# Performance work log

Measured on AMD Instinct MI355X. Metric: run time of the kernel, lower is better.

Reference implementation:

```python
import jax, jax.numpy as jnp
import numpy as np

NEG_SLOPE = 0.01  # torch LeakyReLU default


def lrelu(x):
    return jnp.where(x >= 0, x, NEG_SLOPE * x)


def rgcn_layer(x, edge_index, edge_type, W_rel, W_root, b_rgcn):
    """PyG RGCNConv (no bases/blocks, aggr='mean'):
    out = x @ root + bias + sum_r mean_{j in N_r(i)}(x_j) @ W_r
    Single fused gather/segment_sum over relation-interleaved segment ids."""
    N, D = x.shape
    R = W_rel.shape[0]
    src, dst = edge_index[0], edge_index[1]
    seg = dst * R + edge_type  # interleave relation into segment id
    summed = jax.ops.segment_sum(x[src], seg, num_segments=N * R).reshape(N, R, D)
    cnt = jax.ops.segment_sum(jnp.ones(edge_type.shape, x.dtype), seg, num_segments=N * R).reshape(N, R)
    mean = summed / jnp.maximum(cnt, 1.0)[..., None]  # [N, R, D]
    return x @ W_root + b_rgcn + jnp.einsum('nrd,rde->ne', mean, W_rel)


def setup_inputs() -> dict:
    key = jax.random.key(0)
    N, E, D = 100_000, 3_200_000, 128
    q = D // 4
    ks = jax.random.split(key, 24)
    s = 0.02
    inp = {
        'des': jax.random.normal(ks[0], (N, 768), jnp.float32),
        'tweet': jax.random.normal(ks[1], (N, 768), jnp.float32),
        'prop': jax.random.normal(ks[2], (N, 14), jnp.float32),
        'edge_index': jax.random.randint(ks[3], (2, E), 0, N),
        'edge_type': jax.random.randint(ks[4], (E,), 0, 2),
        # feature encoders
        'W_des': jax.random.normal(ks[5], (768, q), jnp.float32) * s,
        'b_des': jnp.zeros((q,), jnp.float32),
        'W_tweet': jax.random.normal(ks[6], (768, q), jnp.float32) * s,
        'b_tweet': jnp.zeros((q,), jnp.float32),
        'W_prop': jax.random.normal(ks[7], (14, q), jnp.float32) * s,
        'b_prop': jnp.zeros((q,), jnp.float32),
        'W_in': jax.random.normal(ks[8], (3 * q, D), jnp.float32) * s,
        'b_in': jnp.zeros((D,), jnp.float32),
        # shared RGCNConv weights (applied twice)
        'W_rel': jax.random.normal(ks[9], (2, D, D), jnp.float32) * s,
        'W_root': jax.random.normal(ks[10], (D, D), jnp.float32) * s,
        'b_rgcn': jnp.zeros((D,), jnp.float32),
        # output head
        'W_o1': jax.random.normal(ks[11], (D, D), jnp.float32) * s,
        'b_o1': jnp.zeros((D,), jnp.float32),
        'W_o2': jax.random.normal(ks[12], (D, 2), jnp.float32) * s,
        'b_o2': jnp.zeros((2,), jnp.float32),
    }
    return inp


def reference(des, tweet, prop, edge_index, edge_type,
              W_des, b_des, W_tweet, b_tweet, W_prop, b_prop,
              W_in, b_in, W_rel, W_root, b_rgcn,
              W_o1, b_o1, W_o2, b_o2):
    d = lrelu(des @ W_des + b_des)
    t = lrelu(tweet @ W_tweet + b_tweet)
    p = lrelu(prop @ W_prop + b_prop)
    x = lrelu(jnp.concatenate([d, t, p], axis=1) @ W_in + b_in)
    x = rgcn_layer(x, edge_index, edge_type, W_rel, W_root, b_rgcn)
    # dropout is identity at eval time
    x = rgcn_layer(x, edge_index, edge_type, W_rel, W_root, b_rgcn)
    x = lrelu(x @ W_o1 + b_o1)
    return jax.nn.softmax(x @ W_o2 + b_o2, axis=1)
```

## Files before the change

kernel.cpp:

```cpp
#include <hip/hip_runtime.h>
#include <math.h>

typedef __bf16 bf16;
typedef bf16  v8bf __attribute__((ext_vector_type(8)));
typedef bf16  v2bf __attribute__((ext_vector_type(2)));
typedef float v4f  __attribute__((ext_vector_type(4)));

#define LB __launch_bounds__(256)

static inline int cdiv(int a, int b){ return (a + b - 1) / b; }


__global__ LB void zero_int(int* __restrict__ p, int n){
  int i = blockIdx.x * 256 + threadIdx.x;
  if (i < n) p[i] = 0;
}

__global__ LB void count_edges(const int* __restrict__ ei, const int* __restrict__ et,
                               int* __restrict__ cnt, int E, int R){
  int e = blockIdx.x * 256 + threadIdx.x;
  if (e >= E) return;
  int dst = ei[E + e];
  int ty  = et[e];
  atomicAdd(&cnt[dst * R + ty], 1);
}

__global__ LB void block_sum_k(const int* __restrict__ cnt, int* __restrict__ bsum, int NS){
  __shared__ int sh[256];
  int t = threadIdx.x;
  int base = blockIdx.x * 1024;
  int s = 0;
  for (int i = t; i < 1024; i += 256){ int g = base + i; if (g < NS) s += cnt[g]; }
  sh[t] = s; __syncthreads();
  for (int d = 128; d > 0; d >>= 1){ if (t < d) sh[t] += sh[t + d]; __syncthreads(); }
  if (t == 0) bsum[blockIdx.x] = sh[0];
}

__global__ LB void scan_bsum_k(int* __restrict__ bsum, int nb){
  __shared__ int sh[256];
  int t = threadIdx.x;
  int v = (t < nb) ? bsum[t] : 0;
  sh[t] = v; __syncthreads();
  for (int d = 1; d < 256; d <<= 1){
    int add = (t >= d) ? sh[t - d] : 0;
    __syncthreads();
    sh[t] += add;
    __syncthreads();
  }
  if (t < nb) bsum[t] = sh[t] - v;
}

__global__ LB void scan_scatter_k(const int* __restrict__ cnt, const int* __restrict__ bsum,
                                  int* __restrict__ off, int* __restrict__ cursor,
                                  float* __restrict__ degInv, int NS){
  __shared__ int sh[256];
  int t = threadIdx.x;
  int base = blockIdx.x * 1024 + t * 4;
  int v[4];
  #pragma unroll
  for (int j = 0; j < 4; ++j){ int g = base + j; v[j] = (g < NS) ? cnt[g] : 0; }
  int tsum = v[0] + v[1] + v[2] + v[3];
  sh[t] = tsum; __syncthreads();
  for (int d = 1; d < 256; d <<= 1){
    int add = (t >= d) ? sh[t - d] : 0;
    __syncthreads();
    sh[t] += add;
    __syncthreads();
  }
  int o = bsum[blockIdx.x] + sh[t] - tsum;
  #pragma unroll
  for (int j = 0; j < 4; ++j){
    int g = base + j;
    if (g < NS){
      off[g] = o;
      cursor[g] = o;
      degInv[g] = 1.0f / (float)(v[j] > 0 ? v[j] : 1);
      o += v[j];
      if (g == NS - 1) off[NS] = o;
    }
  }
}

__global__ LB void fill_edges(const int* __restrict__ ei, const int* __restrict__ et,
                              int* __restrict__ cursor, int* __restrict__ srcS, int E, int R){
  int e = blockIdx.x * 256 + threadIdx.x;
  if (e >= E) return;
  int src = ei[e];
  int dst = ei[E + e];
  int ty  = et[e];
  int pos = atomicAdd(&cursor[dst * R + ty], 1);
  srcS[pos] = src;
}


__global__ LB void agg_mean_k(const bf16* __restrict__ X, const int* __restrict__ srcS,
                              const int* __restrict__ off, const float* __restrict__ degInv,
                              bf16* __restrict__ mean, int NS){
  int w = (int)(((size_t)blockIdx.x * blockDim.x + threadIdx.x) >> 6);
  int lane = threadIdx.x & 63;
  if (w >= NS) return;
  int s0 = off[w], s1 = off[w + 1];
  float ax = 0.f, ay = 0.f;
  int i = s0;
  for (; i + 4 <= s1; i += 4){
    int j0 = srcS[i], j1 = srcS[i + 1], j2 = srcS[i + 2], j3 = srcS[i + 3];
    v2bf u0 = *(const v2bf*)(X + (size_t)j0 * 128 + lane * 2);
    v2bf u1 = *(const v2bf*)(X + (size_t)j1 * 128 + lane * 2);
    v2bf u2 = *(const v2bf*)(X + (size_t)j2 * 128 + lane * 2);
    v2bf u3 = *(const v2bf*)(X + (size_t)j3 * 128 + lane * 2);
    ax += (float)u0[0] + (float)u1[0] + (float)u2[0] + (float)u3[0];
    ay += (float)u0[1] + (float)u1[1] + (float)u2[1] + (float)u3[1];
  }
  for (; i < s1; ++i){
    int j = srcS[i];
    v2bf u = *(const v2bf*)(X + (size_t)j * 128 + lane * 2);
    ax += (float)u[0]; ay += (float)u[1];
  }
  float di = degInv[w];
  v2bf o; o[0] = (bf16)(ax * di); o[1] = (bf16)(ay * di);
  *(v2bf*)(mean + (size_t)w * 128 + lane * 2) = o;
}


__global__ LB void prep_bt(const float* __restrict__ W, bf16* __restrict__ BT,
                           int K, int Nc, int KP){
  int idx = blockIdx.x * 256 + threadIdx.x;
  if (idx >= Nc * KP) return;
  int n = idx / KP, k = idx - n * KP;
  BT[idx] = (k < K) ? (bf16)W[(size_t)k * Nc + n] : (bf16)0.f;
}

__global__ LB void prep_stack(const float* __restrict__ Wroot, const float* __restrict__ Wrel,
                              bf16* __restrict__ BT, int D){
  int KP = 3 * D;
  int idx = blockIdx.x * 256 + threadIdx.x;
  if (idx >= D * KP) return;
  int n = idx / KP, k = idx - n * KP;
  float v = (k < D) ? Wroot[(size_t)k * D + n] : Wrel[(size_t)(k - D) * D + n];
  BT[idx] = (bf16)v;
}


template<int BN, bool LRELU, bool DUALA, bool ABF, bool CBF>
__global__ LB void gemm_mfma(const void* __restrict__ Av, int lda,
                             const void* __restrict__ A2v, int lda2, int KA,
                             const bf16* __restrict__ BT, int KP,
                             void* __restrict__ Cv, int ldc,
                             const float* __restrict__ bias,
                             int M, int K){
  __shared__ __align__(16) bf16 As[64][40];
  __shared__ __align__(16) bf16 Bs[BN][40];
  const int t = threadIdx.x;
  const int row0 = blockIdx.x * 64;
  const int col0 = blockIdx.y * BN;
  const int wv = t >> 6, ln = t & 63;
  const int mr = ln & 15, quad = ln >> 4;
  const int sr = t >> 2;
  const int sc = (t & 3) * 8;

  v4f acc[BN / 16];
  #pragma unroll
  for (int f = 0; f < BN / 16; ++f) acc[f] = (v4f)0.f;

  for (int k0 = 0; k0 < KP; k0 += 32){
    {
      int gr = row0 + sr;
      int gk = k0 + sc;
      bool useA2 = DUALA && (k0 >= KA);
      if (ABF){
        const bf16* src;
        if (useA2) src = (const bf16*)A2v + (size_t)gr * lda2 + (gk - KA);
        else       src = (const bf16*)Av  + (size_t)gr * lda  + gk;
        v8bf val;
        if (gr < M && gk + 8 <= K){
          val = *(const v8bf*)src;
        } else {
          #pragma unroll
          for (int j = 0; j < 8; ++j)
            val[j] = (gr < M && gk + j < K) ? src[j] : (bf16)0.f;
        }
        *(v8bf*)&As[sr][sc] = val;
      } else {
        const float* src;
        if (useA2) src = (const float*)A2v + (size_t)gr * lda2 + (gk - KA);
        else       src = (const float*)Av  + (size_t)gr * lda  + gk;
        bf16 tmp[8];
        if (gr < M && gk + 8 <= K){
          float4 f0 = *(const float4*)src;
          float4 f1 = *(const float4*)(src + 4);
          tmp[0]=(bf16)f0.x; tmp[1]=(bf16)f0.y; tmp[2]=(bf16)f0.z; tmp[3]=(bf16)f0.w;
          tmp[4]=(bf16)f1.x; tmp[5]=(bf16)f1.y; tmp[6]=(bf16)f1.z; tmp[7]=(bf16)f1.w;
        } else {
          #pragma unroll
          for (int j = 0; j < 8; ++j)
            tmp[j] = (gr < M && gk + j < K) ? (bf16)src[j] : (bf16)0.f;
        }
        *(v8bf*)&As[sr][sc] = *(v8bf*)tmp;
      }
    }
    if (BN == 64 || t < 128){
      *(v8bf*)&Bs[sr][sc] = *(const v8bf*)&BT[(size_t)(col0 + sr) * KP + k0 + sc];
    }
    __syncthreads();
    v8bf a = *(v8bf*)&As[wv * 16 + mr][quad * 8];
    #pragma unroll
    for (int f = 0; f < BN / 16; ++f){
      v8bf b = *(v8bf*)&Bs[f * 16 + mr][quad * 8];
      acc[f] = __builtin_amdgcn_mfma_f32_16x16x32_bf16(a, b, acc[f], 0, 0, 0);
    }
    __syncthreads();
  }

  #pragma unroll
  for (int f = 0; f < BN / 16; ++f){
    int gc = col0 + f * 16 + mr;
    float bv = bias[gc];
    #pragma unroll
    for (int r = 0; r < 4; ++r){
      int gr = row0 + wv * 16 + quad * 4 + r;
      if (gr < M){
        float v = acc[f][r] + bv;
        if (LRELU) v = (v >= 0.f) ? v : 0.01f * v;
        if (CBF) ((bf16*)Cv)[(size_t)gr * ldc + gc] = (bf16)v;
        else     ((float*)Cv)[(size_t)gr * ldc + gc] = v;
      }
    }
  }
}


__global__ LB void head_softmax(const bf16* __restrict__ H, const float* __restrict__ Wo2,
                                const float* __restrict__ bo2, float* __restrict__ out, int Nn){
  int gtid = blockIdx.x * 256 + threadIdx.x;
  int node = gtid >> 5;
  int lane = gtid & 31;
  if (node >= Nn) return;
  float l0 = 0.f, l1 = 0.f;
  #pragma unroll
  for (int kk = 0; kk < 4; ++kk){
    int k = lane + kk * 32;
    float h = (float)H[(size_t)node * 128 + k];
    l0 = fmaf(h, Wo2[k * 2 + 0], l0);
    l1 = fmaf(h, Wo2[k * 2 + 1], l1);
  }
  #pragma unroll
  for (int m = 16; m >= 1; m >>= 1){
    l0 += __shfl_xor(l0, m, 64);
    l1 += __shfl_xor(l1, m, 64);
  }
  if (lane == 0){
    l0 += bo2[0]; l1 += bo2[1];
    float mx = fmaxf(l0, l1);
    float e0 = __expf(l0 - mx), e1 = __expf(l1 - mx);
    float inv = 1.f / (e0 + e1);
    out[(size_t)node * 2 + 0] = e0 * inv;
    out[(size_t)node * 2 + 1] = e1 * inv;
  }
}


extern "C" void kernel_launch(void* const* d_in, const int* in_sizes, int n_in,
                              void* d_out, int out_size, void* d_ws, size_t ws_size,
                              hipStream_t stream) {
  const float* des    = (const float*)d_in[0];
  const float* tweet  = (const float*)d_in[1];
  const float* prop   = (const float*)d_in[2];
  const int*   ei     = (const int*)d_in[3];
  const int*   et     = (const int*)d_in[4];
  const float* W_des  = (const float*)d_in[5];
  const float* b_des  = (const float*)d_in[6];
  const float* W_tw   = (const float*)d_in[7];
  const float* b_tw   = (const float*)d_in[8];
  const float* W_pr   = (const float*)d_in[9];
  const float* b_pr   = (const float*)d_in[10];
  const float* W_in   = (const float*)d_in[11];
  const float* b_in   = (const float*)d_in[12];
  const float* W_rel  = (const float*)d_in[13];
  const float* W_root = (const float*)d_in[14];
  const float* b_rg   = (const float*)d_in[15];
  const float* W_o1   = (const float*)d_in[16];
  const float* b_o1   = (const float*)d_in[17];
  const float* W_o2   = (const float*)d_in[18];
  const float* b_o2   = (const float*)d_in[19];

  const int Nn = in_sizes[0] / 768;
  const int E  = in_sizes[4];
  const int q  = in_sizes[6];
  const int D  = in_sizes[12];
  const int R  = in_sizes[13] / (D * D);
  const int NS = Nn * R;
  const int K3 = 3 * q;

  char* p = (char*)d_ws;
  auto carve = [&](size_t bytes) -> void* {
    void* r = (void*)p;
    p += (bytes + 255) & ~(size_t)255;
    return r;
  };
  int*   cnt     = (int*)  carve((size_t)NS * 4);
  int*   off     = (int*)  carve((size_t)(NS + 1) * 4);
  int*   cursor  = (int*)  carve((size_t)NS * 4);
  float* degInv  = (float*)carve((size_t)NS * 4);
  int*   bsum    = (int*)  carve(4096 * 4);
  int*   srcS    = (int*)  carve((size_t)E * 4);
  bf16*  bufA    = (bf16*) carve((size_t)Nn * D * 2);
  bf16*  bufB    = (bf16*) carve((size_t)Nn * D * 2);
  bf16*  mean    = (bf16*) carve((size_t)Nn * R * D * 2);
  bf16*  dtp     = mean;
  bf16*  BT_des  = (bf16*) carve((size_t)q * 768 * 2);
  bf16*  BT_tw   = (bf16*) carve((size_t)q * 768 * 2);
  bf16*  BT_pr   = (bf16*) carve((size_t)q * 32 * 2);
  bf16*  BT_in   = (bf16*) carve((size_t)D * K3 * 2);
  bf16*  BT_st   = (bf16*) carve((size_t)D * 3 * D * 2);
  bf16*  BT_o1   = (bf16*) carve((size_t)D * D * 2);

  const int NB1 = cdiv(NS, 1024);

  zero_int<<<cdiv(NS, 256), 256, 0, stream>>>(cnt, NS);
  count_edges<<<cdiv(E, 256), 256, 0, stream>>>(ei, et, cnt, E, R);
  block_sum_k<<<NB1, 256, 0, stream>>>(cnt, bsum, NS);
  scan_bsum_k<<<1, 256, 0, stream>>>(bsum, NB1);
  scan_scatter_k<<<NB1, 256, 0, stream>>>(cnt, bsum, off, cursor, degInv, NS);
  fill_edges<<<cdiv(E, 256), 256, 0, stream>>>(ei, et, cursor, srcS, E, R);

  prep_bt<<<cdiv(q * 768, 256), 256, 0, stream>>>(W_des, BT_des, 768, q, 768);
  prep_bt<<<cdiv(q * 768, 256), 256, 0, stream>>>(W_tw,  BT_tw,  768, q, 768);
  prep_bt<<<cdiv(q * 32, 256), 256, 0, stream>>>(W_pr,  BT_pr,  14,  q, 32);
  prep_bt<<<cdiv(D * K3, 256), 256, 0, stream>>>(W_in,  BT_in,  K3,  D, K3);
  prep_stack<<<cdiv(D * 3 * D, 256), 256, 0, stream>>>(W_root, W_rel, BT_st, D);
  prep_bt<<<cdiv(D * D, 256), 256, 0, stream>>>(W_o1,  BT_o1,  D,   D, D);

  const int gx = cdiv(Nn, 64);

  gemm_mfma<32, true, false, false, true><<<dim3(gx, 1), 256, 0, stream>>>(
      des, 768, nullptr, 0, 0, BT_des, 768, dtp + 0, K3, b_des, Nn, 768);
  gemm_mfma<32, true, false, false, true><<<dim3(gx, 1), 256, 0, stream>>>(
      tweet, 768, nullptr, 0, 0, BT_tw, 768, dtp + q, K3, b_tw, Nn, 768);
  gemm_mfma<32, true, false, false, true><<<dim3(gx, 1), 256, 0, stream>>>(
      prop, 14, nullptr, 0, 0, BT_pr, 32, dtp + 2 * q, K3, b_pr, Nn, 14);

  gemm_mfma<64, true, false, true, true><<<dim3(gx, 2), 256, 0, stream>>>(
      dtp, K3, nullptr, 0, 0, BT_in, K3, bufA, D, b_in, Nn, K3);

  const int aggGrid = cdiv(NS * 64, 256);

  agg_mean_k<<<aggGrid, 256, 0, stream>>>(bufA, srcS, off, degInv, mean, NS);
  gemm_mfma<64, false, true, true, true><<<dim3(gx, 2), 256, 0, stream>>>(
      bufA, D, mean, R * D, D, BT_st, 3 * D, bufB, D, b_rg, Nn, 3 * D);

  agg_mean_k<<<aggGrid, 256, 0, stream>>>(bufB, srcS, off, degInv, mean, NS);
  gemm_mfma<64, false, true, true, true><<<dim3(gx, 2), 256, 0, stream>>>(
      bufB, D, mean, R * D, D, BT_st, 3 * D, bufA, D, b_rg, Nn, 3 * D);

  gemm_mfma<64, true, false, true, true><<<dim3(gx, 2), 256, 0, stream>>>(
      bufA, D, nullptr, 0, 0, BT_o1, D, bufB, D, b_o1, Nn, D);
  head_softmax<<<cdiv(Nn * 32, 256), 256, 0, stream>>>(bufB, W_o2, b_o2, (float*)d_out, Nn);
}
```

Baseline: 1.429 ms.

## Build CSR via two-level bucket partition instead of global atomics

Replaces the count/scan/fill CSR construction, which does random global atomics per edge, with a two-pass radix-style partition. Edges are first bucketed by dst>>9 using shared-memory histograms and staged writes. Each bucket then builds its segment offsets and the sorted src list with shared-memory atomics. This trades the scattered global atomic traffic for extra passes over the edge arrays and more workspace, and it assumes Nn fits in 256 buckets and R*512 segments fit in SPB (R<=2).

Result: faster. 1.190 ms (-16.7%).

```diff
diff --git a/kernel.cpp b/kernel.cpp
--- a/kernel.cpp
+++ b/kernel.cpp
@@ -11,35 +11,39 @@
 static inline int cdiv(int a, int b){ return (a + b - 1) / b; }
 
 
+#define PNB   256
+#define CHUNK 4096
+#define SPB   1024
+
 __global__ LB void zero_int(int* __restrict__ p, int n){
   int i = blockIdx.x * 256 + threadIdx.x;
   if (i < n) p[i] = 0;
 }
 
-__global__ LB void count_edges(const int* __restrict__ ei, const int* __restrict__ et,
-                               int* __restrict__ cnt, int E, int R){
-  int e = blockIdx.x * 256 + threadIdx.x;
-  if (e >= E) return;
-  int dst = ei[E + e];
-  int ty  = et[e];
-  atomicAdd(&cnt[dst * R + ty], 1);
-}
-
-__global__ LB void block_sum_k(const int* __restrict__ cnt, int* __restrict__ bsum, int NS){
+__global__ LB void bucket_count_k(const int* __restrict__ ei, int* __restrict__ gCnt, int E){
+  __shared__ int lh[PNB];
+  int t = threadIdx.x;
+  int base = blockIdx.x * CHUNK;
+  for (int i = t; i < PNB; i += 256) lh[i] = 0;
+  __syncthreads();
+  #pragma unroll
+  for (int j = 0; j < 16; ++j){
+    int i = base + t + j * 256;
+    if (i < E){
+      int d = ei[E + i];
+      atomicAdd(&lh[d >> 9], 1);
+    }
+  }
+  __syncthreads();
+  for (int i = t; i < PNB; i += 256) if (lh[i]) atomicAdd(&gCnt[i], lh[i]);
+}
+
+__global__ LB void bucket_scan_k(const int* __restrict__ gCnt, int* __restrict__ bucketBase,
+                                 int* __restrict__ gCur, int* __restrict__ off,
+                                 int NBk, int E, int NS){
   __shared__ int sh[256];
   int t = threadIdx.x;
-  int base = blockIdx.x * 1024;
-  int s = 0;
-  for (int i = t; i < 1024; i += 256){ int g = base + i; if (g < NS) s += cnt[g]; }
-  sh[t] = s; __syncthreads();
-  for (int d = 128; d > 0; d >>= 1){ if (t < d) sh[t] += sh[t + d]; __syncthreads(); }
-  if (t == 0) bsum[blockIdx.x] = sh[0];
-}
-
-__global__ LB void scan_bsum_k(int* __restrict__ bsum, int nb){
-  __shared__ int sh[256];
-  int t = threadIdx.x;
-  int v = (t < nb) ? bsum[t] : 0;
+  int v = (t < NBk) ? gCnt[t] : 0;
   sh[t] = v; __syncthreads();
   for (int d = 1; d < 256; d <<= 1){
     int add = (t >= d) ? sh[t - d] : 0;
@@ -47,49 +51,120 @@
     sh[t] += add;
     __syncthreads();
   }
-  if (t < nb) bsum[t] = sh[t] - v;
-}
-
-__global__ LB void scan_scatter_k(const int* __restrict__ cnt, const int* __restrict__ bsum,
-                                  int* __restrict__ off, int* __restrict__ cursor,
-                                  float* __restrict__ degInv, int NS){
-  __shared__ int sh[256];
+  int excl = sh[t] - v;
+  if (t < NBk){ bucketBase[t] = excl; gCur[t] = excl; }
+  if (t == 0){ bucketBase[NBk] = E; off[NS] = E; }
+}
+
+__global__ LB void partition_k(const int* __restrict__ ei, const int* __restrict__ et,
+                               int* __restrict__ gCur,
+                               int* __restrict__ partSrc, int* __restrict__ partSeg,
+                               int E, int R){
+  __shared__ int lh[PNB];
+  __shared__ int lbase[PNB];
+  __shared__ int gb[PNB];
+  __shared__ int stageSrc[CHUNK];
+  __shared__ int stageSeg[CHUNK];
   int t = threadIdx.x;
-  int base = blockIdx.x * 1024 + t * 4;
-  int v[4];
-  #pragma unroll
-  for (int j = 0; j < 4; ++j){ int g = base + j; v[j] = (g < NS) ? cnt[g] : 0; }
-  int tsum = v[0] + v[1] + v[2] + v[3];
-  sh[t] = tsum; __syncthreads();
+  int base = blockIdx.x * CHUNK;
+  int cntE = E - base; if (cntE > CHUNK) cntE = CHUNK;
+  for (int i = t; i < PNB; i += 256) lh[i] = 0;
+  __syncthreads();
+  int seg_[16], src_[16], pk_[16];
+  #pragma unroll
+  for (int j = 0; j < 16; ++j){
+    int i = t + j * 256;
+    if (i < cntE){
+      int e = base + i;
+      int s  = ei[e];
+      int d  = ei[E + e];
+      int ty = et[e];
+      seg_[j] = d * R + ty;
+      src_[j] = s;
+      int b = d >> 9;
+      int r = atomicAdd(&lh[b], 1);
+      pk_[j] = (b << 16) | r;
+    } else pk_[j] = -1;
+  }
+  __syncthreads();
+  int v = lh[t];
+  lbase[t] = v; __syncthreads();
   for (int d = 1; d < 256; d <<= 1){
-    int add = (t >= d) ? sh[t - d] : 0;
-    __syncthreads();
-    sh[t] += add;
-    __syncthreads();
-  }
-  int o = bsum[blockIdx.x] + sh[t] - tsum;
+    int add = (t >= d) ? lbase[t - d] : 0;
+    __syncthreads();
+    lbase[t] += add;
+    __syncthreads();
+  }
+  int excl = lbase[t] - v;
+  int gbase = 0;
+  if (v > 0) gbase = atomicAdd(&gCur[t], v);
+  __syncthreads();
+  lbase[t] = excl;
+  gb[t] = gbase;
+  __syncthreads();
+  #pragma unroll
+  for (int j = 0; j < 16; ++j){
+    if (pk_[j] >= 0){
+      int b = pk_[j] >> 16, r = pk_[j] & 0xffff;
+      int pos = lbase[b] + r;
+      stageSrc[pos] = src_[j];
+      stageSeg[pos] = seg_[j];
+    }
+  }
+  __syncthreads();
+  for (int i = t; i < cntE; i += 256){
+    int sg = stageSeg[i];
+    int b = (sg / R) >> 9;
+    int g = gb[b] + (i - lbase[b]);
+    partSeg[g] = sg;
+    partSrc[g] = stageSrc[i];
+  }
+}
+
+__global__ LB void bucket_csr_k(const int* __restrict__ partSrc, const int* __restrict__ partSeg,
+                                const int* __restrict__ bucketBase,
+                                int* __restrict__ off, float* __restrict__ degInv,
+                                int* __restrict__ srcS, int NS, int R){
+  __shared__ int lh[SPB];
+  __shared__ int lsc[256];
+  int b = blockIdx.x, t = threadIdx.x;
+  int s0 = bucketBase[b], s1 = bucketBase[b + 1];
+  int segBase = b * SPB;
+  for (int i = t; i < SPB; i += 256) lh[i] = 0;
+  __syncthreads();
+  for (int i = s0 + t; i < s1; i += 256)
+    atomicAdd(&lh[partSeg[i] - segBase], 1);
+  __syncthreads();
+  int base4 = t * 4;
+  int v0 = lh[base4], v1 = lh[base4 + 1], v2 = lh[base4 + 2], v3 = lh[base4 + 3];
+  int tsum = v0 + v1 + v2 + v3;
+  lsc[t] = tsum; __syncthreads();
+  for (int d = 1; d < 256; d <<= 1){
+    int add = (t >= d) ? lsc[t - d] : 0;
+    __syncthreads();
+    lsc[t] += add;
+    __syncthreads();
+  }
+  int o = lsc[t] - tsum;
+  int cs[4] = {v0, v1, v2, v3};
   #pragma unroll
   for (int j = 0; j < 4; ++j){
-    int g = base + j;
+    int ls = base4 + j;
+    int g = segBase + ls;
+    int c = cs[j];
     if (g < NS){
-      off[g] = o;
-      cursor[g] = o;
-      degInv[g] = 1.0f / (float)(v[j] > 0 ? v[j] : 1);
-      o += v[j];
-      if (g == NS - 1) off[NS] = o;
-    }
-  }
-}
-
-__global__ LB void fill_edges(const int* __restrict__ ei, const int* __restrict__ et,
-                              int* __restrict__ cursor, int* __restrict__ srcS, int E, int R){
-  int e = blockIdx.x * 256 + threadIdx.x;
-  if (e >= E) return;
-  int src = ei[e];
-  int dst = ei[E + e];
-  int ty  = et[e];
-  int pos = atomicAdd(&cursor[dst * R + ty], 1);
-  srcS[pos] = src;
+      off[g] = s0 + o;
+      degInv[g] = 1.0f / (float)(c > 0 ? c : 1);
+    }
+    lh[ls] = o;
+    o += c;
+  }
+  __syncthreads();
+  for (int i = s0 + t; i < s1; i += 256){
+    int sg = partSeg[i];
+    int r = atomicAdd(&lh[sg - segBase], 1);
+    srcS[s0 + r] = partSrc[i];
+  }
 }
 
 
@@ -290,6 +365,7 @@
   const int R  = in_sizes[13] / (D * D);
   const int NS = Nn * R;
   const int K3 = 3 * q;
+  const int NB = cdiv(Nn, 512);
 
   char* p = (char*)d_ws;
   auto carve = [&](size_t bytes) -> void* {
@@ -297,12 +373,14 @@
     p += (bytes + 255) & ~(size_t)255;
     return r;
   };
-  int*   cnt     = (int*)  carve((size_t)NS * 4);
   int*   off     = (int*)  carve((size_t)(NS + 1) * 4);
-  int*   cursor  = (int*)  carve((size_t)NS * 4);
   float* degInv  = (float*)carve((size_t)NS * 4);
-  int*   bsum    = (int*)  carve(4096 * 4);
   int*   srcS    = (int*)  carve((size_t)E * 4);
+  int*   gCnt    = (int*)  carve(PNB * 4);
+  int*   gCur    = (int*)  carve(PNB * 4);
+  int*   bktBase = (int*)  carve((PNB + 1) * 4);
+  int*   partSrc = (int*)  carve((size_t)E * 4);
+  int*   partSeg = (int*)  carve((size_t)E * 4);
   bf16*  bufA    = (bf16*) carve((size_t)Nn * D * 2);
   bf16*  bufB    = (bf16*) carve((size_t)Nn * D * 2);
   bf16*  mean    = (bf16*) carve((size_t)Nn * R * D * 2);
@@ -314,14 +392,11 @@
   bf16*  BT_st   = (bf16*) carve((size_t)D * 3 * D * 2);
   bf16*  BT_o1   = (bf16*) carve((size_t)D * D * 2);
 
-  const int NB1 = cdiv(NS, 1024);
-
-  zero_int<<<cdiv(NS, 256), 256, 0, stream>>>(cnt, NS);
-  count_edges<<<cdiv(E, 256), 256, 0, stream>>>(ei, et, cnt, E, R);
-  block_sum_k<<<NB1, 256, 0, stream>>>(cnt, bsum, NS);
-  scan_bsum_k<<<1, 256, 0, stream>>>(bsum, NB1);
-  scan_scatter_k<<<NB1, 256, 0, stream>>>(cnt, bsum, off, cursor, degInv, NS);
-  fill_edges<<<cdiv(E, 256), 256, 0, stream>>>(ei, et, cursor, srcS, E, R);
+  zero_int<<<1, 256, 0, stream>>>(gCnt, PNB);
+  bucket_count_k<<<cdiv(E, CHUNK), 256, 0, stream>>>(ei, gCnt, E);
+  bucket_scan_k<<<1, 256, 0, stream>>>(gCnt, bktBase, gCur, off, NB, E, NS);
+  partition_k<<<cdiv(E, CHUNK), 256, 0, stream>>>(ei, et, gCur, partSrc, partSeg, E, R);
+  bucket_csr_k<<<NB, 256, 0, stream>>>(partSrc, partSeg, bktBase, off, degInv, srcS, NS, R);
 
   prep_bt<<<cdiv(q * 768, 256), 256, 0, stream>>>(W_des, BT_des, 768, q, 768);
   prep_bt<<<cdiv(q * 768, 256), 256, 0, stream>>>(W_tw,  BT_tw,  768, q, 768);
```
